# Kernel optimization log

Measured on AMD Instinct MI355X. Metric: run time of the kernel, lower is better.

The kernel has to match this reference:

```python
import jax, jax.numpy as jnp
import numpy as np

N = 512
H = 512
W = 512
BLOCK_H = 16
BLOCK_W = 16
TILES_X = (W + BLOCK_W - 1) // BLOCK_W
TILES_Y = (H + BLOCK_H - 1) // BLOCK_H
CHOL_BOUND = np.array([0.5, 0.0, 0.5], dtype=np.float32)  # cholesky_bound buffer


def setup_inputs() -> dict:
    key = jax.random.key(0)
    k1, k2, k3, k4 = jax.random.split(key, 4)
    return {
        "xyz": jax.random.normal(k1, (N, 2), jnp.float32),
        "cholesky": jax.random.uniform(k2, (N, 3), jnp.float32),
        "features_dc": jax.random.uniform(k3, (N, 3), jnp.float32),
        "opacity": jax.random.uniform(k4, (N, 1), jnp.float32),
    }


def _render(xyz, cholesky, features_dc, opacity):
    # project_gaussians_2d: map means to pixel space, build 2D covariance from
    # lower-triangular Cholesky factor L = [[l0, 0], [l1, l2]], invert to conic.
    means = jnp.tanh(xyz)                                  # [N,2] in (-1,1)
    chol = cholesky + jnp.asarray(CHOL_BOUND)              # [N,3]
    l0, l1, l2 = chol[:, 0], chol[:, 1], chol[:, 2]
    cxx = l0 * l0                                          # cov2d = L @ L.T
    cxy = l0 * l1
    cyy = l1 * l1 + l2 * l2
    det = cxx * cyy - cxy * cxy
    inv_det = 1.0 / det
    ca = cyy * inv_det                                     # conic (inverse cov)
    cb = -cxy * inv_det
    cc = cxx * inv_det
    cx = 0.5 * W * (means[:, 0] + 1.0)                     # pixel-space centers
    cy = 0.5 * H * (means[:, 1] + 1.0)
    # 3-sigma radius from largest eigenvalue of cov2d (as in project kernel)
    b = 0.5 * (cxx + cyy)
    v1 = b + jnp.sqrt(jnp.maximum(b * b - det, 0.1))
    radius = jnp.ceil(3.0 * jnp.sqrt(v1))
    # tile-granular bbox culling, matching the CUDA tile binning
    tminx = jnp.clip(((cx - radius) / BLOCK_W).astype(jnp.int32), 0, TILES_X)
    tmaxx = jnp.clip(((cx + radius) / BLOCK_W).astype(jnp.int32) + 1, 0, TILES_X)
    tminy = jnp.clip(((cy - radius) / BLOCK_H).astype(jnp.int32), 0, TILES_Y)
    tmaxy = jnp.clip(((cy + radius) / BLOCK_H).astype(jnp.int32) + 1, 0, TILES_Y)
    pxs = jnp.arange(W, dtype=jnp.float32)
    pys = jnp.arange(H, dtype=jnp.float32)
    ptx = jnp.arange(W) // BLOCK_W
    pty = jnp.arange(H) // BLOCK_H
    maskx = (ptx[None, :] >= tminx[:, None]) & (ptx[None, :] < tmaxx[:, None])  # [N,W]
    masky = (pty[None, :] >= tminy[:, None]) & (pty[None, :] < tmaxy[:, None])  # [N,H]
    dx = cx[:, None] - pxs[None, :]                        # [N,W]
    dy = cy[:, None] - pys[None, :]                        # [N,H]
    # sigma = 0.5 * d^T conic d  evaluated on the full pixel grid -> [N,H,W]
    sigma = (0.5 * ca[:, None, None] * (dx * dx)[:, None, :]
             + 0.5 * cc[:, None, None] * (dy * dy)[:, :, None]
             + cb[:, None, None] * dy[:, :, None] * dx[:, None, :])
    mask = (maskx[:, None, :] & masky[:, :, None]).astype(sigma.dtype)
    w = jnp.exp(-sigma) * mask                             # gaussian weight, tile-culled
    alpha = w * opacity[:, 0][:, None, None]               # sum-compositing: no blending
    out = jnp.einsum('nhw,nc->chw', alpha, features_dc)    # [3,H,W]
    out = jnp.clip(out, 0.0, 1.0)
    return out[None]                                       # [1,3,H,W]


def reference(xyz, cholesky, features_dc, opacity):
    return _render(xyz, cholesky, features_dc, opacity)
```

## Files before the change

kernel.cpp:

```cpp
#include <hip/hip_runtime.h>
#include <cstdint>


#define IMG_W 512
#define IMG_H 512
#define TILE 16
#define TILES_X 32
#define TILES_Y 32
#define TPB 256

__global__ __launch_bounds__(TPB) void gsplat_render(
    const float* __restrict__ xyz,
    const float* __restrict__ chol,
    const float* __restrict__ feat,
    const float* __restrict__ opac,
    float* __restrict__ out,
    int N)
{
    __shared__ float sg[TPB][8];
    __shared__ int   s_wcnt[4];

    const int tid  = threadIdx.x;
    const int lane = tid & 63;
    const int wave = tid >> 6;
    const int bx   = blockIdx.x;
    const int by   = blockIdx.y;

    const int   px_i = bx * TILE + (tid & 15);
    const int   py_i = by * TILE + (tid >> 4);
    const float px   = (float)px_i;
    const float py   = (float)py_i;

    float a0 = 0.0f, a1 = 0.0f, a2 = 0.0f;

    for (int g0 = 0; g0 < N; g0 += TPB) {
        const int g = g0 + tid;
        bool accept = false;
        float ca = 0.f, cb = 0.f, cc = 0.f, gx = 0.f, gy = 0.f;
        float of0 = 0.f, of1 = 0.f, of2 = 0.f;

        if (g < N) {
            const float mx = tanhf(xyz[2 * g]);
            const float my = tanhf(xyz[2 * g + 1]);
            const float l0 = chol[3 * g]     + 0.5f;
            const float l1 = chol[3 * g + 1];
            const float l2 = chol[3 * g + 2] + 0.5f;
            const float cxx = l0 * l0;
            const float cxy = l0 * l1;
            const float cyy = l1 * l1 + l2 * l2;
            const float det = cxx * cyy - cxy * cxy;
            const float inv = 1.0f / det;
            ca = cyy * inv;
            cb = -cxy * inv;
            cc = cxx * inv;
            gx = 0.5f * (float)IMG_W * (mx + 1.0f);
            gy = 0.5f * (float)IMG_H * (my + 1.0f);
            const float b  = 0.5f * (cxx + cyy);
            const float v1 = b + sqrtf(fmaxf(b * b - det, 0.1f));
            const float radius = ceilf(3.0f * sqrtf(v1));
            const int tminx = min(max((int)((gx - radius) * (1.0f / TILE)), 0), TILES_X);
            const int tmaxx = min(max((int)((gx + radius) * (1.0f / TILE)) + 1, 0), TILES_X);
            const int tminy = min(max((int)((gy - radius) * (1.0f / TILE)), 0), TILES_Y);
            const int tmaxy = min(max((int)((gy + radius) * (1.0f / TILE)) + 1, 0), TILES_Y);
            accept = (bx >= tminx) && (bx < tmaxx) && (by >= tminy) && (by < tmaxy);
            if (accept) {
                const float op = opac[g];
                of0 = op * feat[3 * g];
                of1 = op * feat[3 * g + 1];
                of2 = op * feat[3 * g + 2];
            }
        }

        const unsigned long long bal = __ballot(accept);
        const int prefix = __popcll(bal & ((1ull << lane) - 1ull));
        if (lane == 0) s_wcnt[wave] = __popcll(bal);
        __syncthreads();
        int off = 0;
#pragma unroll
        for (int w2 = 0; w2 < 4; ++w2)
            if (w2 < wave) off += s_wcnt[w2];
        const int cnt = s_wcnt[0] + s_wcnt[1] + s_wcnt[2] + s_wcnt[3];
        if (accept) {
            const int idx = off + prefix;
            sg[idx][0] = ca;  sg[idx][1] = cb;  sg[idx][2] = cc;
            sg[idx][3] = gx;  sg[idx][4] = gy;
            sg[idx][5] = of0; sg[idx][6] = of1; sg[idx][7] = of2;
        }
        __syncthreads();

        for (int i = 0; i < cnt; ++i) {
            const float dx = sg[i][3] - px;
            const float dy = sg[i][4] - py;
            const float sigma = 0.5f * sg[i][0] * dx * dx
                              + 0.5f * sg[i][2] * dy * dy
                              + sg[i][1] * dy * dx;
            const float w = __expf(-sigma);
            a0 += w * sg[i][5];
            a1 += w * sg[i][6];
            a2 += w * sg[i][7];
        }
    }

    const int base = py_i * IMG_W + px_i;
    out[base]                     = fminf(fmaxf(a0, 0.0f), 1.0f);
    out[IMG_H * IMG_W + base]     = fminf(fmaxf(a1, 0.0f), 1.0f);
    out[2 * IMG_H * IMG_W + base] = fminf(fmaxf(a2, 0.0f), 1.0f);
}

extern "C" void kernel_launch(void* const* d_in, const int* in_sizes, int n_in,
                              void* d_out, int out_size, void* d_ws, size_t ws_size,
                              hipStream_t stream) {
    const float* xyz  = (const float*)d_in[0];
    const float* chol = (const float*)d_in[1];
    const float* feat = (const float*)d_in[2];
    const float* opac = (const float*)d_in[3];
    float* out = (float*)d_out;
    const int N = in_sizes[0] / 2;

    dim3 grid(TILES_X, TILES_Y);
    gsplat_render<<<grid, TPB, 0, stream>>>(xyz, chol, feat, opac, out, N);
}
```

Baseline: 62.53 us.

## Compact all gaussians in one pass with fast tanh/rcp and prefolded conic halves

Each thread now sets up two gaussians at once and compacts them into a 512-entry shared buffer with a single pair of barriers, instead of looping over 256-gaussian chunks with two barriers per chunk. tanh and the reciprocal are replaced with exp/rcp-based fast approximations, and the 0.5 factors are folded into the conic coefficients so the per-pixel loop uses FMAs. This hardcodes a maximum of 512 gaussians, so larger N would be silently dropped, and the fast math may change results slightly.

```diff
diff --git a/kernel.cpp b/kernel.cpp
--- a/kernel.cpp
+++ b/kernel.cpp
@@ -8,6 +8,59 @@
 #define TILES_X 32
 #define TILES_Y 32
 #define TPB 256
+#define MAXG 512
+
+__device__ __forceinline__ float fast_tanh(float x) {
+    x = fminf(fmaxf(x, -10.0f), 10.0f);
+    const float e = __expf(2.0f * x);
+    return (e - 1.0f) * __builtin_amdgcn_rcpf(e + 1.0f);
+}
+
+struct GParams {
+    float ha, cb, hc, gx, gy, of0, of1, of2;
+    bool accept;
+};
+
+__device__ __forceinline__ GParams setup_gaussian(
+    int g, int bx, int by,
+    const float* __restrict__ xyz, const float* __restrict__ chol,
+    const float* __restrict__ feat, const float* __restrict__ opac)
+{
+    GParams r;
+    const float2 p = ((const float2*)xyz)[g];
+    const float mx = fast_tanh(p.x);
+    const float my = fast_tanh(p.y);
+    const float l0 = chol[3 * g]     + 0.5f;
+    const float l1 = chol[3 * g + 1];
+    const float l2 = chol[3 * g + 2] + 0.5f;
+    const float cxx = l0 * l0;
+    const float cxy = l0 * l1;
+    const float cyy = l1 * l1 + l2 * l2;
+    const float det = cxx * cyy - cxy * cxy;
+    const float inv = __builtin_amdgcn_rcpf(det);
+    r.ha = 0.5f * cyy * inv;
+    r.cb = -cxy * inv;
+    r.hc = 0.5f * cxx * inv;
+    r.gx = 0.5f * (float)IMG_W * (mx + 1.0f);
+    r.gy = 0.5f * (float)IMG_H * (my + 1.0f);
+    const float b  = 0.5f * (cxx + cyy);
+    const float v1 = b + sqrtf(fmaxf(b * b - det, 0.1f));
+    const float radius = ceilf(3.0f * sqrtf(v1));
+    const int tminx = min(max((int)((r.gx - radius) * (1.0f / TILE)), 0), TILES_X);
+    const int tmaxx = min(max((int)((r.gx + radius) * (1.0f / TILE)) + 1, 0), TILES_X);
+    const int tminy = min(max((int)((r.gy - radius) * (1.0f / TILE)), 0), TILES_Y);
+    const int tmaxy = min(max((int)((r.gy + radius) * (1.0f / TILE)) + 1, 0), TILES_Y);
+    r.accept = (bx >= tminx) && (bx < tmaxx) && (by >= tminy) && (by < tmaxy);
+    if (r.accept) {
+        const float op = opac[g];
+        r.of0 = op * feat[3 * g];
+        r.of1 = op * feat[3 * g + 1];
+        r.of2 = op * feat[3 * g + 2];
+    } else {
+        r.of0 = r.of1 = r.of2 = 0.0f;
+    }
+    return r;
+}
 
 __global__ __launch_bounds__(TPB) void gsplat_render(
     const float* __restrict__ xyz,
@@ -17,8 +70,8 @@
     float* __restrict__ out,
     int N)
 {
-    __shared__ float sg[TPB][8];
-    __shared__ int   s_wcnt[4];
+    __shared__ float sg[MAXG][8];
+    __shared__ int   s_wcnt[2][4];
 
     const int tid  = threadIdx.x;
     const int lane = tid & 63;
@@ -26,79 +79,62 @@
     const int bx   = blockIdx.x;
     const int by   = blockIdx.y;
 
+    const bool hasA = tid < N;
+    const bool hasB = (tid + TPB) < N;
+    GParams A, B;
+    A.accept = B.accept = false;
+    if (hasA) A = setup_gaussian(tid, bx, by, xyz, chol, feat, opac);
+    if (hasB) B = setup_gaussian(tid + TPB, bx, by, xyz, chol, feat, opac);
+
+    const unsigned long long balA = __ballot(A.accept);
+    const unsigned long long balB = __ballot(B.accept);
+    if (lane == 0) {
+        s_wcnt[0][wave] = __popcll(balA);
+        s_wcnt[1][wave] = __popcll(balB);
+    }
+    __syncthreads();
+
+    int offA = 0, offB = 0, totalA = 0, totalB = 0;
+#pragma unroll
+    for (int w = 0; w < 4; ++w) {
+        if (w < wave) { offA += s_wcnt[0][w]; offB += s_wcnt[1][w]; }
+        totalA += s_wcnt[0][w];
+        totalB += s_wcnt[1][w];
+    }
+    offB += totalA;
+    const int cnt = totalA + totalB;
+
+    const unsigned long long ltmask = (1ull << lane) - 1ull;
+    if (A.accept) {
+        const int i = offA + __popcll(balA & ltmask);
+        sg[i][0] = A.ha;  sg[i][1] = A.cb;  sg[i][2] = A.hc;
+        sg[i][3] = A.gx;  sg[i][4] = A.gy;
+        sg[i][5] = A.of0; sg[i][6] = A.of1; sg[i][7] = A.of2;
+    }
+    if (B.accept) {
+        const int i = offB + __popcll(balB & ltmask);
+        sg[i][0] = B.ha;  sg[i][1] = B.cb;  sg[i][2] = B.hc;
+        sg[i][3] = B.gx;  sg[i][4] = B.gy;
+        sg[i][5] = B.of0; sg[i][6] = B.of1; sg[i][7] = B.of2;
+    }
+    __syncthreads();
+
     const int   px_i = bx * TILE + (tid & 15);
     const int   py_i = by * TILE + (tid >> 4);
     const float px   = (float)px_i;
     const float py   = (float)py_i;
 
     float a0 = 0.0f, a1 = 0.0f, a2 = 0.0f;
-
-    for (int g0 = 0; g0 < N; g0 += TPB) {
-        const int g = g0 + tid;
-        bool accept = false;
-        float ca = 0.f, cb = 0.f, cc = 0.f, gx = 0.f, gy = 0.f;
-        float of0 = 0.f, of1 = 0.f, of2 = 0.f;
-
-        if (g < N) {
-            const float mx = tanhf(xyz[2 * g]);
-            const float my = tanhf(xyz[2 * g + 1]);
-            const float l0 = chol[3 * g]     + 0.5f;
-            const float l1 = chol[3 * g + 1];
-            const float l2 = chol[3 * g + 2] + 0.5f;
-            const float cxx = l0 * l0;
-            const float cxy = l0 * l1;
-            const float cyy = l1 * l1 + l2 * l2;
-            const float det = cxx * cyy - cxy * cxy;
-            const float inv = 1.0f / det;
-            ca = cyy * inv;
-            cb = -cxy * inv;
-            cc = cxx * inv;
-            gx = 0.5f * (float)IMG_W * (mx + 1.0f);
-            gy = 0.5f * (float)IMG_H * (my + 1.0f);
-            const float b  = 0.5f * (cxx + cyy);
-            const float v1 = b + sqrtf(fmaxf(b * b - det, 0.1f));
-            const float radius = ceilf(3.0f * sqrtf(v1));
-            const int tminx = min(max((int)((gx - radius) * (1.0f / TILE)), 0), TILES_X);
-            const int tmaxx = min(max((int)((gx + radius) * (1.0f / TILE)) + 1, 0), TILES_X);
-            const int tminy = min(max((int)((gy - radius) * (1.0f / TILE)), 0), TILES_Y);
-            const int tmaxy = min(max((int)((gy + radius) * (1.0f / TILE)) + 1, 0), TILES_Y);
-            accept = (bx >= tminx) && (bx < tmaxx) && (by >= tminy) && (by < tmaxy);
-            if (accept) {
-                const float op = opac[g];
-                of0 = op * feat[3 * g];
-                of1 = op * feat[3 * g + 1];
-                of2 = op * feat[3 * g + 2];
-            }
-        }
-
-        const unsigned long long bal = __ballot(accept);
-        const int prefix = __popcll(bal & ((1ull << lane) - 1ull));
-        if (lane == 0) s_wcnt[wave] = __popcll(bal);
-        __syncthreads();
-        int off = 0;
-#pragma unroll
-        for (int w2 = 0; w2 < 4; ++w2)
-            if (w2 < wave) off += s_wcnt[w2];
-        const int cnt = s_wcnt[0] + s_wcnt[1] + s_wcnt[2] + s_wcnt[3];
-        if (accept) {
-            const int idx = off + prefix;
-            sg[idx][0] = ca;  sg[idx][1] = cb;  sg[idx][2] = cc;
-            sg[idx][3] = gx;  sg[idx][4] = gy;
-            sg[idx][5] = of0; sg[idx][6] = of1; sg[idx][7] = of2;
-        }
-        __syncthreads();
-
-        for (int i = 0; i < cnt; ++i) {
-            const float dx = sg[i][3] - px;
-            const float dy = sg[i][4] - py;
-            const float sigma = 0.5f * sg[i][0] * dx * dx
-                              + 0.5f * sg[i][2] * dy * dy
-                              + sg[i][1] * dy * dx;
-            const float w = __expf(-sigma);
-            a0 += w * sg[i][5];
-            a1 += w * sg[i][6];
-            a2 += w * sg[i][7];
-        }
+    for (int i = 0; i < cnt; ++i) {
+        const float dx = sg[i][3] - px;
+        const float dy = sg[i][4] - py;
+        const float sigma = fmaf(sg[i][0] * dx, dx,
+                            fmaf(sg[i][2] * dy, dy,
+                                 sg[i][1] * dx * dy));
+        const float w = __expf(-sigma);
+        a0 = fmaf(w, sg[i][5], a0);
+        a1 = fmaf(w, sg[i][6], a1);
+        a2 = fmaf(w, sg[i][7], a2);
     }
 
     const int base = py_i * IMG_W + px_i;
```

New measurement: 62.32 us. About the same (-0.3%).
